# Kernel optimization log

Hardware: AMD Instinct MI355X
Metric: run time of the kernel (lower is better)

The kernel has to match this reference:

```python
import jax, jax.numpy as jnp
import numpy as np

N_TOKEN = 267735
D_EMBED = 1024
D_PROJ = 1024
DIV_VAL = 4
CUTOFF_ENDS = [0, 20000, 40000, 200000, N_TOKEN]
EMB_SCALE = D_PROJ ** 0.5
INIT_STD = 0.02


def setup_inputs() -> dict:
    key = jax.random.key(0)
    ks = jax.random.split(key, 9)
    inp = jax.random.randint(ks[0], (4, 4096), 0, N_TOKEN, dtype=jnp.int32)
    out = {"inp": inp}
    for i in range(4):
        l, r = CUTOFF_ENDS[i], CUTOFF_ENDS[i + 1]
        d_i = D_EMBED // DIV_VAL ** i  # 1024, 256, 64, 16
        tbl = jax.random.normal(ks[1 + i], (r - l, d_i), dtype=jnp.float32)
        # padding_idx=1: row 1 is zero-initialized in torch nn.Embedding
        tbl = tbl.at[1].set(0.0)
        out[f"emb{i}"] = tbl
        out[f"proj{i}"] = jax.random.normal(ks[5 + i], (D_PROJ, d_i), dtype=jnp.float32) * INIT_STD
    return out


def reference(inp, emb0, emb1, emb2, emb3, proj0, proj1, proj2, proj3):
    tables = [emb0, emb1, emb2, emb3]
    projs = [proj0, proj1, proj2, proj3]
    flat = inp.reshape(-1)                                  # [N]
    out = jnp.zeros((flat.shape[0], D_PROJ), dtype=emb0.dtype)
    for i in range(4):
        l, r = CUTOFF_ENDS[i], CUTOFF_ENDS[i + 1]
        mask = (flat >= l) & (flat < r)                     # [N] bool
        local = jnp.clip(flat - l, 0, r - l - 1)            # in-range local idx
        e_i = tables[i][local]                              # [N, d_i] gather
        p_i = jnp.einsum('nd,pd->np', e_i, projs[i])        # [N, D_PROJ]
        out = out + jnp.where(mask[:, None], p_i, 0.0)      # scatter-by-mask
    out = out * EMB_SCALE
    return out.reshape(*inp.shape, D_PROJ)
```

## Files before the change

### kernel.cpp

```cpp
#include <hip/hip_runtime.h>
#include <hip/hip_bf16.h>

#define DPROJ 1024

typedef float  f32x4  __attribute__((ext_vector_type(4)));
typedef short  bf16x8 __attribute__((ext_vector_type(8)));

__device__ __forceinline__ unsigned pk2(float a, float b) {
    __hip_bfloat162 h = __float22bfloat162_rn(make_float2(a, b));
    unsigned r; __builtin_memcpy(&r, &h, 4); return r;
}

__device__ __forceinline__ void gll16(const void* g, void* l) {
    __builtin_amdgcn_global_load_lds(
        (const __attribute__((address_space(1))) void*)g,
        (__attribute__((address_space(3))) void*)l, 16, 0, 0);
}

__global__ __launch_bounds__(256) void k_prep(
    const int* __restrict__ inp, int n,
    int* __restrict__ cnt, int* __restrict__ lists,
    const float* __restrict__ p0, const float* __restrict__ p1,
    const float* __restrict__ p2, const float* __restrict__ p3,
    short* __restrict__ pb0, short* __restrict__ pb1,
    short* __restrict__ pb2, short* __restrict__ pb3)
{
    const int tid = threadIdx.x;
    const int b   = blockIdx.x;
    const int CB  = (n + 255) >> 8;
    if (b < CB) {
        const int t = b * 256 + tid;
        int c = -1, l = 0;
        if (t < n) {
            const int x = inp[t];
            c = (x >= 20000) + (x >= 40000) + (x >= 200000);
            l = x - ((c == 0) ? 0 : (c == 1) ? 20000 : (c == 2) ? 40000 : 200000);
        }
        const int lane = tid & 63;
        int pos = 0;
        #pragma unroll
        for (int cc = 0; cc < 4; ++cc) {
            const unsigned long long mk = __ballot(c == cc);
            if (c == cc) {
                const int lead = __ffsll(mk) - 1;
                int base = 0;
                if (lane == lead) base = atomicAdd(&cnt[cc], (int)__popcll(mk));
                base = __shfl(base, lead);
                pos  = base + (int)__popcll(mk & ((1ull << lane) - 1ull));
            }
        }
        if (t < n) lists[c * n + pos] = (int)(((unsigned)t << 18) | (unsigned)l);
    } else {
        const long g = (long)(b - CB) * 256 + tid;
        if (g < 172032) {
            const float* src; short* dst; long lo;
            if      (g < 131072) { src = p0; dst = pb0; lo = g; }
            else if (g < 163840) { src = p1; dst = pb1; lo = g - 131072; }
            else                 { src = p2; dst = pb2; lo = g - 163840; }
            const float4 a = *(const float4*)(src + lo * 8);
            const float4 d = *(const float4*)(src + lo * 8 + 4);
            uint4 q; q.x = pk2(a.x, a.y); q.y = pk2(a.z, a.w);
                     q.z = pk2(d.x, d.y); q.w = pk2(d.z, d.w);
            *(uint4*)(dst + lo * 8) = q;
        } else if (g < 176128) {
            const long lo = g - 172032;
            const int col = (int)(lo >> 2), c = (int)(lo & 3);
            uint4 q = (uint4){0u, 0u, 0u, 0u};
            if (c < 2) {
                const float* src = p3 + (size_t)col * 16 + c * 8;
                const float4 a = *(const float4*)src;
                const float4 d = *(const float4*)(src + 4);
                q.x = pk2(a.x, a.y); q.y = pk2(a.z, a.w);
                q.z = pk2(d.x, d.y); q.w = pk2(d.z, d.w);
            }
            *(uint4*)(pb3 + (size_t)col * 32 + c * 8) = q;
        }
    }
}

__global__ __launch_bounds__(256) void k_egather(
    const int* __restrict__ cnt, const int* __restrict__ lists, int n,
    const float* __restrict__ e0, const float* __restrict__ e1,
    const float* __restrict__ e2, const float* __restrict__ e3,
    short* __restrict__ ec)
{
    const int c0 = cnt[0], c1 = cnt[1], c2 = cnt[2], c3 = cnt[3];
    const long t0 = (long)c0 * 128;
    const long t1 = t0 + (long)c1 * 32;
    const long t2 = t1 + (long)c2 * 8;
    const long t3 = t2 + (long)c3 * 4;
    const long o1 = (long)c0 * 1024;
    const long o2 = o1 + (long)c1 * 256;
    const long o3 = o2 + (long)c2 * 64;

    const long stride = (long)gridDim.x * 256;
    for (long i = (long)blockIdx.x * 256 + threadIdx.x; i < t3; i += stride) {
        int z, Kp, Kr, lc; long rem, off; const float* emb;
        if (i < t0)      { z = 0; rem = i;      off = 0;  emb = e0; Kp = 1024; Kr = 1024; lc = 7; }
        else if (i < t1) { z = 1; rem = i - t0; off = o1; emb = e1; Kp = 256;  Kr = 256;  lc = 5; }
        else if (i < t2) { z = 2; rem = i - t1; off = o2; emb = e2; Kp = 64;   Kr = 64;   lc = 3; }
        else             { z = 3; rem = i - t2; off = o3; emb = e3; Kp = 32;   Kr = 16;   lc = 2; }
        const int r = (int)(rem >> lc);
        const int c = (int)(rem & ((1 << lc) - 1));
        const int k = c * 8;
        uint4 q = (uint4){0u, 0u, 0u, 0u};
        if (k < Kr) {
            const int loc = lists[z * n + r] & 0x3FFFF;
            const float* src = emb + (size_t)loc * Kr + k;
            const float4 a = *(const float4*)src;
            const float4 d = *(const float4*)(src + 4);
            q.x = pk2(a.x, a.y); q.y = pk2(a.z, a.w);
            q.z = pk2(d.x, d.y); q.w = pk2(d.z, d.w);
        }
        const int gsw = (c & ~3) | ((c ^ ((r >> 1) & 3)) & 3);
        *(uint4*)(ec + off + (size_t)r * Kp + gsw * 8) = q;
    }
}

__global__ __launch_bounds__(256, 6) void k_gemm(
    const int* __restrict__ cnt, const int* __restrict__ lists, int n,
    const short* __restrict__ ec,
    const short* __restrict__ pb0, const short* __restrict__ pb1,
    const short* __restrict__ pb2, const short* __restrict__ pb3,
    float* __restrict__ out)
{
    const int yb = blockIdx.x, z = blockIdx.y, xb = blockIdx.z;
    const int count = cnt[z];
    const int row0  = yb * 64;
    if (row0 >= count) return;

    const int c0 = cnt[0], c1 = cnt[1], c2 = cnt[2];
    const short* pb = (z == 0) ? pb0 : (z == 1) ? pb1 : (z == 2) ? pb2 : pb3;
    const int    Kp = (z == 0) ? 1024 : (z == 1) ? 256 : (z == 2) ? 64 : 32;
    const long eoff = (z == 0) ? 0
                    : (z == 1) ? (long)c0 * 1024
                    : (z == 2) ? (long)c0 * 1024 + (long)c1 * 256
                               : (long)c0 * 1024 + (long)c1 * 256 + (long)c2 * 64;
    const short* ecz  = ec + eoff;
    const int    nt   = Kp >> 5;
    const int    col0 = xb * 128;
    const int*   list = lists + (size_t)z * n;

    __shared__ int   s_tok[64];
    __shared__ short e_s[2][64 * 32];
    __shared__ short p_s[2][4 * 128 * 8];

    const int tid = threadIdx.x;
    if (tid < 64) {
        const int r = row0 + tid;
        s_tok[tid] = (r < count) ? (int)((unsigned)list[r] >> 18) : -1;
    }

    const int wave = tid >> 6, lane = tid & 63;
    const int lm = lane & 15, quad = lane >> 4;

    const short* esrc = ecz + (size_t)(row0 + wave * 16 + (lane >> 2)) * Kp
                            + (lane & 3) * 8;
    short* eb   = &e_s[0][0];
    const int edst = wave * 512;

    const short* psrc0 = pb + (size_t)(col0 +      lane) * Kp + wave * 8;
    const short* psrc1 = pb + (size_t)(col0 + 64 + lane) * Kp + wave * 8;
    short* pbuf_ = &p_s[0][0];
    const int pdst = wave * 1024;

    const int eread = (wave * 16 + lm) * 32 + (quad ^ ((lm >> 1) & 3)) * 8;
    const int pread = quad * 1024 + lm * 8;

    f32x4 acc[8];
    #pragma unroll
    for (int i = 0; i < 8; ++i) acc[i] = (f32x4){0.f, 0.f, 0.f, 0.f};

    gll16(esrc,  eb    + edst);
    gll16(psrc0, pbuf_ + pdst);
    gll16(psrc1, pbuf_ + pdst + 512);
    __syncthreads();

    for (int t = 0; t < nt; ++t) {
        const int cur = t & 1;
        if (t + 1 < nt) {
            const int kb = (t + 1) * 32;
            const int nb = cur ^ 1;
            gll16(esrc  + kb, eb    + nb * 2048 + edst);
            gll16(psrc0 + kb, pbuf_ + nb * 4096 + pdst);
            gll16(psrc1 + kb, pbuf_ + nb * 4096 + pdst + 512);
        }
        const bf16x8 ebf = *(const bf16x8*)(eb + cur * 2048 + eread);
        const short* pk_ = pbuf_ + cur * 4096 + pread;
        #pragma unroll
        for (int ns = 0; ns < 8; ++ns) {
            bf16x8 pfr = *(const bf16x8*)(pk_ + ns * 128);
            acc[ns] = __builtin_amdgcn_mfma_f32_16x16x32_bf16(pfr, ebf, acc[ns], 0, 0, 0);
        }
        __syncthreads();
    }

    const int tok = s_tok[wave * 16 + lm];
    if (tok >= 0) {
        float* orow = out + (size_t)tok * DPROJ + col0 + quad * 4;
        #pragma unroll
        for (int ns = 0; ns < 8; ++ns) {
            f32x4 v = acc[ns] * 32.f;
            *(f32x4*)(orow + ns * 16) = v;
        }
    }
}

extern "C" void kernel_launch(void* const* d_in, const int* in_sizes, int n_in,
                              void* d_out, int out_size, void* d_ws, size_t ws_size,
                              hipStream_t stream) {
    const int*   inp = (const int*)d_in[0];
    const float* e0  = (const float*)d_in[1];
    const float* p0  = (const float*)d_in[2];
    const float* e1  = (const float*)d_in[3];
    const float* p1  = (const float*)d_in[4];
    const float* e2  = (const float*)d_in[5];
    const float* p2  = (const float*)d_in[6];
    const float* e3  = (const float*)d_in[7];
    const float* p3  = (const float*)d_in[8];
    float* out = (float*)d_out;
    const int n = in_sizes[0];

    char* wsb  = (char*)d_ws;
    int* cnt   = (int*)wsb;
    int* lists = (int*)(wsb + 16);
    size_t off = 16 + (size_t)4 * n * sizeof(int);
    off = (off + 255) & ~(size_t)255;
    short* pb0 = (short*)(wsb + off); off += (size_t)1024 * 1024 * 2;
    short* pb1 = (short*)(wsb + off); off += (size_t)1024 * 256 * 2;
    short* pb2 = (short*)(wsb + off); off += (size_t)1024 * 64 * 2;
    short* pb3 = (short*)(wsb + off); off += (size_t)1024 * 32 * 2;
    short* ec  = (short*)(wsb + off);

    hipMemsetAsync(cnt, 0, 4 * sizeof(int), stream);

    const int CB = (n + 255) >> 8;
    k_prep<<<CB + 688, 256, 0, stream>>>(inp, n, cnt, lists,
                                         p0, p1, p2, p3, pb0, pb1, pb2, pb3);
    k_egather<<<1024, 256, 0, stream>>>(cnt, lists, n, e0, e1, e2, e3, ec);

    dim3 grid((n + 63) / 64, 4, 8);
    k_gemm<<<grid, 256, 0, stream>>>(cnt, lists, n, ec,
                                     pb0, pb1, pb2, pb3, out);
}
```

Before: 228.5 us.

## Make GEMM persistent with atomic tile ticket scheduling across regions

```diff
diff --git a/kernel.cpp b/kernel.cpp
--- a/kernel.cpp
+++ b/kernel.cpp
@@ -118,90 +118,105 @@
 }
 
 __global__ __launch_bounds__(256, 6) void k_gemm(
-    const int* __restrict__ cnt, const int* __restrict__ lists, int n,
+    const int* __restrict__ cnt, int* __restrict__ ticket,
+    const int* __restrict__ lists, int n,
     const short* __restrict__ ec,
     const short* __restrict__ pb0, const short* __restrict__ pb1,
     const short* __restrict__ pb2, const short* __restrict__ pb3,
     float* __restrict__ out)
 {
-    const int yb = blockIdx.x, z = blockIdx.y, xb = blockIdx.z;
-    const int count = cnt[z];
-    const int row0  = yb * 64;
-    if (row0 >= count) return;
-
-    const int c0 = cnt[0], c1 = cnt[1], c2 = cnt[2];
-    const short* pb = (z == 0) ? pb0 : (z == 1) ? pb1 : (z == 2) ? pb2 : pb3;
-    const int    Kp = (z == 0) ? 1024 : (z == 1) ? 256 : (z == 2) ? 64 : 32;
-    const long eoff = (z == 0) ? 0
-                    : (z == 1) ? (long)c0 * 1024
-                    : (z == 2) ? (long)c0 * 1024 + (long)c1 * 256
-                               : (long)c0 * 1024 + (long)c1 * 256 + (long)c2 * 64;
-    const short* ecz  = ec + eoff;
-    const int    nt   = Kp >> 5;
-    const int    col0 = xb * 128;
-    const int*   list = lists + (size_t)z * n;
+    const int c0 = cnt[0], c1 = cnt[1], c2 = cnt[2], c3 = cnt[3];
+    const int T0 = ((c0 + 63) >> 6) << 3, T1 = ((c1 + 63) >> 6) << 3;
+    const int T2 = ((c2 + 63) >> 6) << 3, T3 = ((c3 + 63) >> 6) << 3;
+    const int ntile = T0 + T1 + T2 + T3;
+    const long o1 = (long)c0 * 1024;
+    const long o2 = o1 + (long)c1 * 256;
+    const long o3 = o2 + (long)c2 * 64;
 
     __shared__ int   s_tok[64];
     __shared__ short e_s[2][64 * 32];
     __shared__ short p_s[2][4 * 128 * 8];
-
-    const int tid = threadIdx.x;
-    if (tid < 64) {
-        const int r = row0 + tid;
-        s_tok[tid] = (r < count) ? (int)((unsigned)list[r] >> 18) : -1;
-    }
-
+    __shared__ int   s_ticket;
+
+    const int tid  = threadIdx.x;
     const int wave = tid >> 6, lane = tid & 63;
     const int lm = lane & 15, quad = lane >> 4;
 
-    const short* esrc = ecz + (size_t)(row0 + wave * 16 + (lane >> 2)) * Kp
-                            + (lane & 3) * 8;
-    short* eb   = &e_s[0][0];
-    const int edst = wave * 512;
-
-    const short* psrc0 = pb + (size_t)(col0 +      lane) * Kp + wave * 8;
-    const short* psrc1 = pb + (size_t)(col0 + 64 + lane) * Kp + wave * 8;
-    short* pbuf_ = &p_s[0][0];
-    const int pdst = wave * 1024;
-
-    const int eread = (wave * 16 + lm) * 32 + (quad ^ ((lm >> 1) & 3)) * 8;
-    const int pread = quad * 1024 + lm * 8;
-
-    f32x4 acc[8];
-    #pragma unroll
-    for (int i = 0; i < 8; ++i) acc[i] = (f32x4){0.f, 0.f, 0.f, 0.f};
-
-    gll16(esrc,  eb    + edst);
-    gll16(psrc0, pbuf_ + pdst);
-    gll16(psrc1, pbuf_ + pdst + 512);
-    __syncthreads();
-
-    for (int t = 0; t < nt; ++t) {
-        const int cur = t & 1;
-        if (t + 1 < nt) {
-            const int kb = (t + 1) * 32;
-            const int nb = cur ^ 1;
-            gll16(esrc  + kb, eb    + nb * 2048 + edst);
-            gll16(psrc0 + kb, pbuf_ + nb * 4096 + pdst);
-            gll16(psrc1 + kb, pbuf_ + nb * 4096 + pdst + 512);
-        }
-        const bf16x8 ebf = *(const bf16x8*)(eb + cur * 2048 + eread);
-        const short* pk_ = pbuf_ + cur * 4096 + pread;
+    for (;;) {
+        if (tid == 0) s_ticket = atomicAdd(ticket, 1);
+        __syncthreads();
+        const int i = s_ticket;
+        if (i >= ntile) return;
+
+        int z, r;
+        if      (i < T0)           { z = 0; r = i; }
+        else if (i < T0 + T1)      { z = 1; r = i - T0; }
+        else if (i < T0 + T1 + T2) { z = 2; r = i - T0 - T1; }
+        else                       { z = 3; r = i - T0 - T1 - T2; }
+        const int yb = r >> 3, xb = r & 7;
+        const int count = (z == 0) ? c0 : (z == 1) ? c1 : (z == 2) ? c2 : c3;
+        const int Kp    = (z == 0) ? 1024 : (z == 1) ? 256 : (z == 2) ? 64 : 32;
+        const short* pb = (z == 0) ? pb0 : (z == 1) ? pb1 : (z == 2) ? pb2 : pb3;
+        const long eoff = (z == 0) ? 0 : (z == 1) ? o1 : (z == 2) ? o2 : o3;
+        const int row0 = yb * 64, col0 = xb * 128;
+        const int nt   = Kp >> 5;
+        const int* list = lists + (size_t)z * n;
+
+        if (tid < 64) {
+            const int rr = row0 + tid;
+            s_tok[tid] = (rr < count) ? (int)((unsigned)list[rr] >> 18) : -1;
+        }
+
+        int erow = row0 + wave * 16 + (lane >> 2);
+        if (erow >= count) erow = count - 1;
+        const short* esrc = ec + eoff + (size_t)erow * Kp + (lane & 3) * 8;
+        short* eb = &e_s[0][0];
+        const int edst = wave * 512;
+
+        const short* psrc0 = pb + (size_t)(col0 +      lane) * Kp + wave * 8;
+        const short* psrc1 = pb + (size_t)(col0 + 64 + lane) * Kp + wave * 8;
+        short* pbuf_ = &p_s[0][0];
+        const int pdst = wave * 1024;
+
+        const int eread = (wave * 16 + lm) * 32 + (quad ^ ((lm >> 1) & 3)) * 8;
+        const int pread = quad * 1024 + lm * 8;
+
+        f32x4 acc[8];
         #pragma unroll
-        for (int ns = 0; ns < 8; ++ns) {
-            bf16x8 pfr = *(const bf16x8*)(pk_ + ns * 128);
-            acc[ns] = __builtin_amdgcn_mfma_f32_16x16x32_bf16(pfr, ebf, acc[ns], 0, 0, 0);
-        }
+        for (int a = 0; a < 8; ++a) acc[a] = (f32x4){0.f, 0.f, 0.f, 0.f};
+
+        gll16(esrc,  eb    + edst);
+        gll16(psrc0, pbuf_ + pdst);
+        gll16(psrc1, pbuf_ + pdst + 512);
         __syncthreads();
-    }
-
-    const int tok = s_tok[wave * 16 + lm];
-    if (tok >= 0) {
-        float* orow = out + (size_t)tok * DPROJ + col0 + quad * 4;
-        #pragma unroll
-        for (int ns = 0; ns < 8; ++ns) {
-            f32x4 v = acc[ns] * 32.f;
-            *(f32x4*)(orow + ns * 16) = v;
+
+        for (int t = 0; t < nt; ++t) {
+            const int cur = t & 1;
+            if (t + 1 < nt) {
+                const int kb = (t + 1) * 32;
+                const int nb = cur ^ 1;
+                gll16(esrc  + kb, eb    + nb * 2048 + edst);
+                gll16(psrc0 + kb, pbuf_ + nb * 4096 + pdst);
+                gll16(psrc1 + kb, pbuf_ + nb * 4096 + pdst + 512);
+            }
+            const bf16x8 ebf = *(const bf16x8*)(eb + cur * 2048 + eread);
+            const short* pk_ = pbuf_ + cur * 4096 + pread;
+            #pragma unroll
+            for (int ns = 0; ns < 8; ++ns) {
+                bf16x8 pfr = *(const bf16x8*)(pk_ + ns * 128);
+                acc[ns] = __builtin_amdgcn_mfma_f32_16x16x32_bf16(pfr, ebf, acc[ns], 0, 0, 0);
+            }
+            __syncthreads();
+        }
+
+        const int tok = s_tok[wave * 16 + lm];
+        if (tok >= 0) {
+            float* orow = out + (size_t)tok * DPROJ + col0 + quad * 4;
+            #pragma unroll
+            for (int ns = 0; ns < 8; ++ns) {
+                f32x4 v = acc[ns] * 32.f;
+                *(f32x4*)(orow + ns * 16) = v;
+            }
         }
     }
 }
@@ -222,9 +237,10 @@
     const int n = in_sizes[0];
 
     char* wsb  = (char*)d_ws;
-    int* cnt   = (int*)wsb;
-    int* lists = (int*)(wsb + 16);
-    size_t off = 16 + (size_t)4 * n * sizeof(int);
+    int* cnt    = (int*)wsb;
+    int* ticket = cnt + 4;
+    int* lists  = (int*)(wsb + 32);
+    size_t off = 32 + (size_t)4 * n * sizeof(int);
     off = (off + 255) & ~(size_t)255;
     short* pb0 = (short*)(wsb + off); off += (size_t)1024 * 1024 * 2;
     short* pb1 = (short*)(wsb + off); off += (size_t)1024 * 256 * 2;
@@ -232,14 +248,13 @@
     short* pb3 = (short*)(wsb + off); off += (size_t)1024 * 32 * 2;
     short* ec  = (short*)(wsb + off);
 
-    hipMemsetAsync(cnt, 0, 4 * sizeof(int), stream);
+    hipMemsetAsync(cnt, 0, 32, stream);
 
     const int CB = (n + 255) >> 8;
     k_prep<<<CB + 688, 256, 0, stream>>>(inp, n, cnt, lists,
                                          p0, p1, p2, p3, pb0, pb1, pb2, pb3);
     k_egather<<<1024, 256, 0, stream>>>(cnt, lists, n, e0, e1, e2, e3, ec);
 
-    dim3 grid((n + 63) / 64, 4, 8);
-    k_gemm<<<grid, 256, 0, stream>>>(cnt, lists, n, ec,
+    k_gemm<<<1536, 256, 0, stream>>>(cnt, ticket, lists, n, ec,
                                      pb0, pb1, pb2, pb3, out);
 }
```

Result: slower. 241.4 us (+5.7%).

## Replace LDS-staged GEMM with direct register-loaded MFMA tiles

Applied to the files above, without the earlier changes.

```diff
diff --git a/kernel.cpp b/kernel.cpp
--- a/kernel.cpp
+++ b/kernel.cpp
@@ -9,12 +9,6 @@
 __device__ __forceinline__ unsigned pk2(float a, float b) {
     __hip_bfloat162 h = __float22bfloat162_rn(make_float2(a, b));
     unsigned r; __builtin_memcpy(&r, &h, 4); return r;
-}
-
-__device__ __forceinline__ void gll16(const void* g, void* l) {
-    __builtin_amdgcn_global_load_lds(
-        (const __attribute__((address_space(1))) void*)g,
-        (__attribute__((address_space(3))) void*)l, 16, 0, 0);
 }
 
 __global__ __launch_bounds__(256) void k_prep(
@@ -112,12 +106,11 @@
             q.x = pk2(a.x, a.y); q.y = pk2(a.z, a.w);
             q.z = pk2(d.x, d.y); q.w = pk2(d.z, d.w);
         }
-        const int gsw = (c & ~3) | ((c ^ ((r >> 1) & 3)) & 3);
-        *(uint4*)(ec + off + (size_t)r * Kp + gsw * 8) = q;
-    }
-}
-
-__global__ __launch_bounds__(256, 6) void k_gemm(
+        *(uint4*)(ec + off + (size_t)r * Kp + c * 8) = q;
+    }
+}
+
+__global__ __launch_bounds__(256, 4) void k_gemm(
     const int* __restrict__ cnt, const int* __restrict__ lists, int n,
     const short* __restrict__ ec,
     const short* __restrict__ pb0, const short* __restrict__ pb1,
@@ -125,85 +118,91 @@
     float* __restrict__ out)
 {
     const int yb = blockIdx.x, z = blockIdx.y, xb = blockIdx.z;
-    const int count = cnt[z];
+    const int c0 = cnt[0], c1 = cnt[1], c2 = cnt[2], c3 = cnt[3];
+    const int count = (z == 0) ? c0 : (z == 1) ? c1 : (z == 2) ? c2 : c3;
     const int row0  = yb * 64;
     if (row0 >= count) return;
 
-    const int c0 = cnt[0], c1 = cnt[1], c2 = cnt[2];
     const short* pb = (z == 0) ? pb0 : (z == 1) ? pb1 : (z == 2) ? pb2 : pb3;
     const int    Kp = (z == 0) ? 1024 : (z == 1) ? 256 : (z == 2) ? 64 : 32;
     const long eoff = (z == 0) ? 0
                     : (z == 1) ? (long)c0 * 1024
                     : (z == 2) ? (long)c0 * 1024 + (long)c1 * 256
                                : (long)c0 * 1024 + (long)c1 * 256 + (long)c2 * 64;
-    const short* ecz  = ec + eoff;
-    const int    nt   = Kp >> 5;
-    const int    col0 = xb * 128;
-    const int*   list = lists + (size_t)z * n;
-
-    __shared__ int   s_tok[64];
-    __shared__ short e_s[2][64 * 32];
-    __shared__ short p_s[2][4 * 128 * 8];
-
-    const int tid = threadIdx.x;
-    if (tid < 64) {
-        const int r = row0 + tid;
-        s_tok[tid] = (r < count) ? (int)((unsigned)list[r] >> 18) : -1;
-    }
-
+    const int nt    = Kp >> 5;
+    const int* list = lists + (size_t)z * n;
+
+    const int tid  = threadIdx.x;
     const int wave = tid >> 6, lane = tid & 63;
     const int lm = lane & 15, quad = lane >> 4;
-
-    const short* esrc = ecz + (size_t)(row0 + wave * 16 + (lane >> 2)) * Kp
-                            + (lane & 3) * 8;
-    short* eb   = &e_s[0][0];
-    const int edst = wave * 512;
-
-    const short* psrc0 = pb + (size_t)(col0 +      lane) * Kp + wave * 8;
-    const short* psrc1 = pb + (size_t)(col0 + 64 + lane) * Kp + wave * 8;
-    short* pbuf_ = &p_s[0][0];
-    const int pdst = wave * 1024;
-
-    const int eread = (wave * 16 + lm) * 32 + (quad ^ ((lm >> 1) & 3)) * 8;
-    const int pread = quad * 1024 + lm * 8;
-
-    f32x4 acc[8];
-    #pragma unroll
-    for (int i = 0; i < 8; ++i) acc[i] = (f32x4){0.f, 0.f, 0.f, 0.f};
-
-    gll16(esrc,  eb    + edst);
-    gll16(psrc0, pbuf_ + pdst);
-    gll16(psrc1, pbuf_ + pdst + 512);
-    __syncthreads();
-
-    for (int t = 0; t < nt; ++t) {
-        const int cur = t & 1;
-        if (t + 1 < nt) {
-            const int kb = (t + 1) * 32;
-            const int nb = cur ^ 1;
-            gll16(esrc  + kb, eb    + nb * 2048 + edst);
-            gll16(psrc0 + kb, pbuf_ + nb * 4096 + pdst);
-            gll16(psrc1 + kb, pbuf_ + nb * 4096 + pdst + 512);
-        }
-        const bf16x8 ebf = *(const bf16x8*)(eb + cur * 2048 + eread);
-        const short* pk_ = pbuf_ + cur * 4096 + pread;
-        #pragma unroll
-        for (int ns = 0; ns < 8; ++ns) {
-            bf16x8 pfr = *(const bf16x8*)(pk_ + ns * 128);
-            acc[ns] = __builtin_amdgcn_mfma_f32_16x16x32_bf16(pfr, ebf, acc[ns], 0, 0, 0);
-        }
-        __syncthreads();
-    }
-
-    const int tok = s_tok[wave * 16 + lm];
-    if (tok >= 0) {
-        float* orow = out + (size_t)tok * DPROJ + col0 + quad * 4;
-        #pragma unroll
-        for (int ns = 0; ns < 8; ++ns) {
-            f32x4 v = acc[ns] * 32.f;
-            *(f32x4*)(orow + ns * 16) = v;
-        }
-    }
+    const int colA = xb * 128 + wave * 32;
+
+    int tk0, tk1, tk2, tk3;
+    {
+        const int r0 = row0 + lm, r1 = r0 + 16, r2 = r0 + 32, r3 = r0 + 48;
+        tk0 = (r0 < count) ? (int)((unsigned)list[r0] >> 18) : -1;
+        tk1 = (r1 < count) ? (int)((unsigned)list[r1] >> 18) : -1;
+        tk2 = (r2 < count) ? (int)((unsigned)list[r2] >> 18) : -1;
+        tk3 = (r3 < count) ? (int)((unsigned)list[r3] >> 18) : -1;
+    }
+
+    const short* pa0 = pb + (size_t)(colA +      lm) * Kp + quad * 8;
+    const short* pa1 = pb + (size_t)(colA + 16 + lm) * Kp + quad * 8;
+    const int rc = count - 1;
+    int e0r = row0 + lm,      e1r = row0 + 16 + lm;
+    int e2r = row0 + 32 + lm, e3r = row0 + 48 + lm;
+    if (e0r > rc) e0r = rc;  if (e1r > rc) e1r = rc;
+    if (e2r > rc) e2r = rc;  if (e3r > rc) e3r = rc;
+    const short* pe0 = ec + eoff + (size_t)e0r * Kp + quad * 8;
+    const short* pe1 = ec + eoff + (size_t)e1r * Kp + quad * 8;
+    const short* pe2 = ec + eoff + (size_t)e2r * Kp + quad * 8;
+    const short* pe3 = ec + eoff + (size_t)e3r * Kp + quad * 8;
+
+    f32x4 acc00 = {0,0,0,0}, acc01 = {0,0,0,0};
+    f32x4 acc10 = {0,0,0,0}, acc11 = {0,0,0,0};
+    f32x4 acc20 = {0,0,0,0}, acc21 = {0,0,0,0};
+    f32x4 acc30 = {0,0,0,0}, acc31 = {0,0,0,0};
+
+    #define LD8(p) (*(const bf16x8*)(p))
+    bf16x8 a0 = LD8(pa0), a1 = LD8(pa1);
+    bf16x8 b0 = LD8(pe0), b1 = LD8(pe1), b2 = LD8(pe2), b3 = LD8(pe3);
+
+    for (int t = 0; t + 1 < nt; ++t) {
+        pa0 += 32; pa1 += 32; pe0 += 32; pe1 += 32; pe2 += 32; pe3 += 32;
+        bf16x8 na0 = LD8(pa0), na1 = LD8(pa1);
+        bf16x8 nb0 = LD8(pe0), nb1 = LD8(pe1), nb2 = LD8(pe2), nb3 = LD8(pe3);
+        acc00 = __builtin_amdgcn_mfma_f32_16x16x32_bf16(a0, b0, acc00, 0, 0, 0);
+        acc01 = __builtin_amdgcn_mfma_f32_16x16x32_bf16(a1, b0, acc01, 0, 0, 0);
+        acc10 = __builtin_amdgcn_mfma_f32_16x16x32_bf16(a0, b1, acc10, 0, 0, 0);
+        acc11 = __builtin_amdgcn_mfma_f32_16x16x32_bf16(a1, b1, acc11, 0, 0, 0);
+        acc20 = __builtin_amdgcn_mfma_f32_16x16x32_bf16(a0, b2, acc20, 0, 0, 0);
+        acc21 = __builtin_amdgcn_mfma_f32_16x16x32_bf16(a1, b2, acc21, 0, 0, 0);
+        acc30 = __builtin_amdgcn_mfma_f32_16x16x32_bf16(a0, b3, acc30, 0, 0, 0);
+        acc31 = __builtin_amdgcn_mfma_f32_16x16x32_bf16(a1, b3, acc31, 0, 0, 0);
+        a0 = na0; a1 = na1; b0 = nb0; b1 = nb1; b2 = nb2; b3 = nb3;
+    }
+    acc00 = __builtin_amdgcn_mfma_f32_16x16x32_bf16(a0, b0, acc00, 0, 0, 0);
+    acc01 = __builtin_amdgcn_mfma_f32_16x16x32_bf16(a1, b0, acc01, 0, 0, 0);
+    acc10 = __builtin_amdgcn_mfma_f32_16x16x32_bf16(a0, b1, acc10, 0, 0, 0);
+    acc11 = __builtin_amdgcn_mfma_f32_16x16x32_bf16(a1, b1, acc11, 0, 0, 0);
+    acc20 = __builtin_amdgcn_mfma_f32_16x16x32_bf16(a0, b2, acc20, 0, 0, 0);
+    acc21 = __builtin_amdgcn_mfma_f32_16x16x32_bf16(a1, b2, acc21, 0, 0, 0);
+    acc30 = __builtin_amdgcn_mfma_f32_16x16x32_bf16(a0, b3, acc30, 0, 0, 0);
+    acc31 = __builtin_amdgcn_mfma_f32_16x16x32_bf16(a1, b3, acc31, 0, 0, 0);
+    #undef LD8
+
+    const int cbase = colA + quad * 4;
+    #define ST(tk, A0, A1)                                               \
+        if ((tk) >= 0) {                                                 \
+            float* orow = out + (size_t)(tk) * DPROJ + cbase;            \
+            *(f32x4*)(orow)      = A0 * 32.f;                            \
+            *(f32x4*)(orow + 16) = A1 * 32.f;                            \
+        }
+    ST(tk0, acc00, acc01)
+    ST(tk1, acc10, acc11)
+    ST(tk2, acc20, acc21)
+    ST(tk3, acc30, acc31)
+    #undef ST
 }
 
 extern "C" void kernel_launch(void* const* d_in, const int* in_sizes, int n_in,
@@ -223,8 +222,8 @@
 
     char* wsb  = (char*)d_ws;
     int* cnt   = (int*)wsb;
-    int* lists = (int*)(wsb + 16);
-    size_t off = 16 + (size_t)4 * n * sizeof(int);
+    int* lists = (int*)(wsb + 32);
+    size_t off = 32 + (size_t)4 * n * sizeof(int);
     off = (off + 255) & ~(size_t)255;
     short* pb0 = (short*)(wsb + off); off += (size_t)1024 * 1024 * 2;
     short* pb1 = (short*)(wsb + off); off += (size_t)1024 * 256 * 2;
@@ -232,7 +231,7 @@
     short* pb3 = (short*)(wsb + off); off += (size_t)1024 * 32 * 2;
     short* ec  = (short*)(wsb + off);
 
-    hipMemsetAsync(cnt, 0, 4 * sizeof(int), stream);
+    hipMemsetAsync(cnt, 0, 32, stream);
 
     const int CB = (n + 255) >> 8;
     k_prep<<<CB + 688, 256, 0, stream>>>(inp, n, cnt, lists,
```

New measurement: 265.2 us. 1.16x slower.

## Enlarge GEMM tile to 64x256 with 4x4 MFMA blocking and compact grid

Applied to the files above, without the earlier changes.

```diff
diff --git a/kernel.cpp b/kernel.cpp
--- a/kernel.cpp
+++ b/kernel.cpp
@@ -112,96 +112,130 @@
             q.x = pk2(a.x, a.y); q.y = pk2(a.z, a.w);
             q.z = pk2(d.x, d.y); q.w = pk2(d.z, d.w);
         }
-        const int gsw = (c & ~3) | ((c ^ ((r >> 1) & 3)) & 3);
-        *(uint4*)(ec + off + (size_t)r * Kp + gsw * 8) = q;
-    }
-}
-
-__global__ __launch_bounds__(256, 6) void k_gemm(
+        *(uint4*)(ec + off + (size_t)r * Kp + c * 8) = q;
+    }
+}
+
+__global__ __launch_bounds__(256, 2) void k_gemm(
     const int* __restrict__ cnt, const int* __restrict__ lists, int n,
     const short* __restrict__ ec,
     const short* __restrict__ pb0, const short* __restrict__ pb1,
     const short* __restrict__ pb2, const short* __restrict__ pb3,
     float* __restrict__ out)
 {
-    const int yb = blockIdx.x, z = blockIdx.y, xb = blockIdx.z;
-    const int count = cnt[z];
-    const int row0  = yb * 64;
-    if (row0 >= count) return;
-
-    const int c0 = cnt[0], c1 = cnt[1], c2 = cnt[2];
+    const int c0 = cnt[0], c1 = cnt[1], c2 = cnt[2], c3 = cnt[3];
+    const int T0 = (c0 + 63) >> 6, T1 = (c1 + 63) >> 6;
+    const int T2 = (c2 + 63) >> 6, T3 = (c3 + 63) >> 6;
+    const int xb = (int)blockIdx.x & 3;
+    const int gy = (int)blockIdx.x >> 2;
+    if (gy >= T0 + T1 + T2 + T3) return;
+
+    int z, yb;
+    if      (gy < T0)           { z = 0; yb = gy; }
+    else if (gy < T0 + T1)      { z = 1; yb = gy - T0; }
+    else if (gy < T0 + T1 + T2) { z = 2; yb = gy - T0 - T1; }
+    else                        { z = 3; yb = gy - T0 - T1 - T2; }
+
+    const int count = (z == 0) ? c0 : (z == 1) ? c1 : (z == 2) ? c2 : c3;
+    const int Kp    = (z == 0) ? 1024 : (z == 1) ? 256 : (z == 2) ? 64 : 32;
     const short* pb = (z == 0) ? pb0 : (z == 1) ? pb1 : (z == 2) ? pb2 : pb3;
-    const int    Kp = (z == 0) ? 1024 : (z == 1) ? 256 : (z == 2) ? 64 : 32;
     const long eoff = (z == 0) ? 0
                     : (z == 1) ? (long)c0 * 1024
                     : (z == 2) ? (long)c0 * 1024 + (long)c1 * 256
                                : (long)c0 * 1024 + (long)c1 * 256 + (long)c2 * 64;
-    const short* ecz  = ec + eoff;
-    const int    nt   = Kp >> 5;
-    const int    col0 = xb * 128;
-    const int*   list = lists + (size_t)z * n;
-
-    __shared__ int   s_tok[64];
-    __shared__ short e_s[2][64 * 32];
-    __shared__ short p_s[2][4 * 128 * 8];
+    const int nt   = Kp >> 5;
+    const int row0 = yb * 64, col0 = xb * 256;
+    const int* list = lists + (size_t)z * n;
+
+    __shared__ __align__(16) short e_s[2 * 2048];
+    __shared__ __align__(16) short p_s[2 * 8192];
 
     const int tid = threadIdx.x;
-    if (tid < 64) {
-        const int r = row0 + tid;
-        s_tok[tid] = (r < count) ? (int)((unsigned)list[r] >> 18) : -1;
-    }
-
     const int wave = tid >> 6, lane = tid & 63;
     const int lm = lane & 15, quad = lane >> 4;
 
-    const short* esrc = ecz + (size_t)(row0 + wave * 16 + (lane >> 2)) * Kp
-                            + (lane & 3) * 8;
-    short* eb   = &e_s[0][0];
-    const int edst = wave * 512;
-
-    const short* psrc0 = pb + (size_t)(col0 +      lane) * Kp + wave * 8;
-    const short* psrc1 = pb + (size_t)(col0 + 64 + lane) * Kp + wave * 8;
-    short* pbuf_ = &p_s[0][0];
-    const int pdst = wave * 1024;
-
-    const int eread = (wave * 16 + lm) * 32 + (quad ^ ((lm >> 1) & 3)) * 8;
-    const int pread = quad * 1024 + lm * 8;
-
-    f32x4 acc[8];
+    int er = row0 + lane; const int rc = count - 1; if (er > rc) er = rc;
+    const short* esrc = ec + eoff + (size_t)er * Kp + wave * 8;
+    const short* ps0 = pb + (size_t)(col0 +       lane) * Kp + wave * 8;
+    const short* ps1 = pb + (size_t)(col0 +  64 + lane) * Kp + wave * 8;
+    const short* ps2 = pb + (size_t)(col0 + 128 + lane) * Kp + wave * 8;
+    const short* ps3 = pb + (size_t)(col0 + 192 + lane) * Kp + wave * 8;
+
+    f32x4 acc[4][4];
     #pragma unroll
-    for (int i = 0; i < 8; ++i) acc[i] = (f32x4){0.f, 0.f, 0.f, 0.f};
-
-    gll16(esrc,  eb    + edst);
-    gll16(psrc0, pbuf_ + pdst);
-    gll16(psrc1, pbuf_ + pdst + 512);
-    __syncthreads();
+    for (int a = 0; a < 4; ++a)
+        #pragma unroll
+        for (int b = 0; b < 4; ++b) acc[a][b] = (f32x4){0.f, 0.f, 0.f, 0.f};
+
+    gll16(esrc, e_s + wave * 512);
+    gll16(ps0,  p_s + wave * 2048);
+    gll16(ps1,  p_s + wave * 2048 + 512);
+    gll16(ps2,  p_s + wave * 2048 + 1024);
+    gll16(ps3,  p_s + wave * 2048 + 1536);
 
     for (int t = 0; t < nt; ++t) {
         const int cur = t & 1;
         if (t + 1 < nt) {
             const int kb = (t + 1) * 32;
             const int nb = cur ^ 1;
-            gll16(esrc  + kb, eb    + nb * 2048 + edst);
-            gll16(psrc0 + kb, pbuf_ + nb * 4096 + pdst);
-            gll16(psrc1 + kb, pbuf_ + nb * 4096 + pdst + 512);
-        }
-        const bf16x8 ebf = *(const bf16x8*)(eb + cur * 2048 + eread);
-        const short* pk_ = pbuf_ + cur * 4096 + pread;
-        #pragma unroll
-        for (int ns = 0; ns < 8; ++ns) {
-            bf16x8 pfr = *(const bf16x8*)(pk_ + ns * 128);
-            acc[ns] = __builtin_amdgcn_mfma_f32_16x16x32_bf16(pfr, ebf, acc[ns], 0, 0, 0);
-        }
-        __syncthreads();
-    }
-
-    const int tok = s_tok[wave * 16 + lm];
-    if (tok >= 0) {
-        float* orow = out + (size_t)tok * DPROJ + col0 + quad * 4;
-        #pragma unroll
-        for (int ns = 0; ns < 8; ++ns) {
-            f32x4 v = acc[ns] * 32.f;
-            *(f32x4*)(orow + ns * 16) = v;
+            gll16(esrc + kb, e_s + nb * 2048 + wave * 512);
+            gll16(ps0  + kb, p_s + nb * 8192 + wave * 2048);
+            gll16(ps1  + kb, p_s + nb * 8192 + wave * 2048 + 512);
+            gll16(ps2  + kb, p_s + nb * 8192 + wave * 2048 + 1024);
+            gll16(ps3  + kb, p_s + nb * 8192 + wave * 2048 + 1536);
+            asm volatile("s_waitcnt vmcnt(5)" ::: "memory");
+        } else {
+            asm volatile("s_waitcnt vmcnt(0)" ::: "memory");
+        }
+        __builtin_amdgcn_s_barrier();
+        __builtin_amdgcn_sched_barrier(0);
+
+        const short* eb = e_s + cur * 2048 + quad * 512 + lm * 8;
+        const short* pa = p_s + cur * 8192 + quad * 2048 + wave * 512 + lm * 8;
+        bf16x8 B0 = *(const bf16x8*)(eb);
+        bf16x8 B1 = *(const bf16x8*)(eb + 128);
+        bf16x8 B2 = *(const bf16x8*)(eb + 256);
+        bf16x8 B3 = *(const bf16x8*)(eb + 384);
+        bf16x8 A0 = *(const bf16x8*)(pa);
+        bf16x8 A1 = *(const bf16x8*)(pa + 128);
+        bf16x8 A2 = *(const bf16x8*)(pa + 256);
+        bf16x8 A3 = *(const bf16x8*)(pa + 384);
+
+        acc[0][0] = __builtin_amdgcn_mfma_f32_16x16x32_bf16(A0, B0, acc[0][0], 0, 0, 0);
+        acc[1][0] = __builtin_amdgcn_mfma_f32_16x16x32_bf16(A1, B0, acc[1][0], 0, 0, 0);
+        acc[2][0] = __builtin_amdgcn_mfma_f32_16x16x32_bf16(A2, B0, acc[2][0], 0, 0, 0);
+        acc[3][0] = __builtin_amdgcn_mfma_f32_16x16x32_bf16(A3, B0, acc[3][0], 0, 0, 0);
+        acc[0][1] = __builtin_amdgcn_mfma_f32_16x16x32_bf16(A0, B1, acc[0][1], 0, 0, 0);
+        acc[1][1] = __builtin_amdgcn_mfma_f32_16x16x32_bf16(A1, B1, acc[1][1], 0, 0, 0);
+        acc[2][1] = __builtin_amdgcn_mfma_f32_16x16x32_bf16(A2, B1, acc[2][1], 0, 0, 0);
+        acc[3][1] = __builtin_amdgcn_mfma_f32_16x16x32_bf16(A3, B1, acc[3][1], 0, 0, 0);
+        acc[0][2] = __builtin_amdgcn_mfma_f32_16x16x32_bf16(A0, B2, acc[0][2], 0, 0, 0);
+        acc[1][2] = __builtin_amdgcn_mfma_f32_16x16x32_bf16(A1, B2, acc[1][2], 0, 0, 0);
+        acc[2][2] = __builtin_amdgcn_mfma_f32_16x16x32_bf16(A2, B2, acc[2][2], 0, 0, 0);
+        acc[3][2] = __builtin_amdgcn_mfma_f32_16x16x32_bf16(A3, B2, acc[3][2], 0, 0, 0);
+        acc[0][3] = __builtin_amdgcn_mfma_f32_16x16x32_bf16(A0, B3, acc[0][3], 0, 0, 0);
+        acc[1][3] = __builtin_amdgcn_mfma_f32_16x16x32_bf16(A1, B3, acc[1][3], 0, 0, 0);
+        acc[2][3] = __builtin_amdgcn_mfma_f32_16x16x32_bf16(A2, B3, acc[2][3], 0, 0, 0);
+        acc[3][3] = __builtin_amdgcn_mfma_f32_16x16x32_bf16(A3, B3, acc[3][3], 0, 0, 0);
+
+        if (t + 1 < nt) {
+            asm volatile("s_waitcnt lgkmcnt(0)" ::: "memory");
+            __builtin_amdgcn_sched_barrier(0);
+            __builtin_amdgcn_s_barrier();
+            __builtin_amdgcn_sched_barrier(0);
+        }
+    }
+
+    const int colW = col0 + wave * 64 + quad * 4;
+    #pragma unroll
+    for (int b = 0; b < 4; ++b) {
+        const int r = row0 + b * 16 + lm;
+        if (r < count) {
+            const int tok = (int)((unsigned)list[r] >> 18);
+            float* orow = out + (size_t)tok * DPROJ + colW;
+            #pragma unroll
+            for (int a = 0; a < 4; ++a)
+                *(f32x4*)(orow + a * 16) = acc[a][b] * 32.f;
         }
     }
 }
@@ -223,8 +257,8 @@
 
     char* wsb  = (char*)d_ws;
     int* cnt   = (int*)wsb;
-    int* lists = (int*)(wsb + 16);
-    size_t off = 16 + (size_t)4 * n * sizeof(int);
+    int* lists = (int*)(wsb + 32);
+    size_t off = 32 + (size_t)4 * n * sizeof(int);
     off = (off + 255) & ~(size_t)255;
     short* pb0 = (short*)(wsb + off); off += (size_t)1024 * 1024 * 2;
     short* pb1 = (short*)(wsb + off); off += (size_t)1024 * 256 * 2;
@@ -232,14 +266,14 @@
     short* pb3 = (short*)(wsb + off); off += (size_t)1024 * 32 * 2;
     short* ec  = (short*)(wsb + off);
 
-    hipMemsetAsync(cnt, 0, 4 * sizeof(int), stream);
+    hipMemsetAsync(cnt, 0, 32, stream);
 
     const int CB = (n + 255) >> 8;
     k_prep<<<CB + 688, 256, 0, stream>>>(inp, n, cnt, lists,
                                          p0, p1, p2, p3, pb0, pb1, pb2, pb3);
     k_egather<<<1024, 256, 0, stream>>>(cnt, lists, n, e0, e1, e2, e3, ec);
 
-    dim3 grid((n + 63) / 64, 4, 8);
-    k_gemm<<<grid, 256, 0, stream>>>(cnt, lists, n, ec,
-                                     pb0, pb1, pb2, pb3, out);
-}
+    const int NT = (n + 63) / 64 + 4;
+    k_gemm<<<NT * 4, 256, 0, stream>>>(cnt, lists, n, ec,
+                                       pb0, pb1, pb2, pb3, out);
+}
```

Result: faster. 224.0 us (-2.0%).
